# Performance work log

Hardware: AMD Instinct MI355X
Metric: run time of the kernel (lower is better)

## Reference

```python
import jax, jax.numpy as jnp
import numpy as np

N_FREQS = 10
EPS = 1e-5

def embed(p):
    # NeRF positional embedding: [p, sin(p*2^0), cos(p*2^0), ..., sin(p*2^9), cos(p*2^9)]
    freqs = 2.0 ** jnp.arange(N_FREQS, dtype=p.dtype)  # [10]
    ang = p[:, :, None] * freqs[None, None, :]          # [N,3,10]
    sc = jnp.stack([jnp.sin(ang), jnp.cos(ang)], axis=-1)  # [N,3,10,2]
    return jnp.concatenate([p, sc.reshape(p.shape[0], -1)], axis=-1)  # [N, 63]

def edge_conv(x, edge_index, w1, b1, w2, b2):
    src, dst = edge_index[0], edge_index[1]
    xi = x[dst]                                # target features [E, F]
    h = jnp.concatenate([xi, x[src] - xi], -1)  # [E, 2F]
    h = jax.nn.relu(h @ w1 + b1) @ w2 + b2      # [E, out]
    n = x.shape[0]
    s = jax.ops.segment_sum(h, dst, num_segments=n)
    cnt = jax.ops.segment_sum(jnp.ones((h.shape[0],), h.dtype), dst, num_segments=n)
    return s / jnp.clip(cnt, 1.0)[:, None]      # mean aggregation

def batch_norm(x, gamma, beta):
    mu = jnp.mean(x, axis=0)
    var = jnp.mean((x - mu) ** 2, axis=0)
    return (x - mu) * jax.lax.rsqrt(var + EPS) * gamma + beta

def distribute_features(features, face_indices, num_vertices):
    n, f = features.shape
    feat = features.reshape(n * 3, f // 3)
    idx = face_indices.reshape(-1)
    vsum = jax.ops.segment_sum(feat, idx, num_segments=num_vertices)
    cnt = jax.ops.segment_sum(jnp.ones((idx.shape[0],), feat.dtype), idx, num_segments=num_vertices)
    vmean = vsum / jnp.clip(cnt, 1.0)[:, None]
    return vmean[idx].reshape(n, f)

def _mlp_params(key, in_dim, out_dim):
    k1, k2, k3, k4 = jax.random.split(key, 4)
    h = 2 * out_dim
    return (jax.random.normal(k1, (2 * in_dim, h), jnp.float32) * (1.0 / np.sqrt(2 * in_dim)),
            jax.random.normal(k2, (h,), jnp.float32) * 0.01,
            jax.random.normal(k3, (h, out_dim), jnp.float32) * (1.0 / np.sqrt(h)),
            jax.random.normal(k4, (out_dim,), jnp.float32) * 0.01)

def setup_inputs() -> dict:
    key = jax.random.key(0)
    ks = jax.random.split(key, 10)
    N, E, V = 100000, 300000, 50000
    inp = {
        'x': jax.random.normal(ks[0], (N, 16), jnp.float32),
        'edge_index': jax.random.randint(ks[1], (2, E), 0, N, jnp.int32),
        'faces': jax.random.randint(ks[2], (N, 3), 0, V, jnp.int32),
        'num_vertices': V,
    }
    dims = [(196, 96), (96, 192), (192, 384), (384, 384), (384, 576)]
    for i, (di, do) in enumerate(dims, start=1):
        w1, b1, w2, b2 = _mlp_params(ks[2 + i], di, do)
        inp[f'gc{i}_w1'], inp[f'gc{i}_b1'], inp[f'gc{i}_w2'], inp[f'gc{i}_b2'] = w1, b1, w2, b2
    for i, d in enumerate([96, 192, 384, 384], start=1):
        inp[f'gamma{i}'] = jnp.ones((d,), jnp.float32)
        inp[f'beta{i}'] = jnp.zeros((d,), jnp.float32)
    return inp

def reference(x, edge_index, faces, num_vertices,
              gc1_w1, gc1_b1, gc1_w2, gc1_b2,
              gc2_w1, gc2_b1, gc2_w2, gc2_b2,
              gc3_w1, gc3_b1, gc3_w2, gc3_b2,
              gc4_w1, gc4_b1, gc4_w2, gc4_b2,
              gc5_w1, gc5_b1, gc5_w2, gc5_b2,
              gamma1, beta1, gamma2, beta2, gamma3, beta3, gamma4, beta4):
    h = jnp.concatenate([embed(x[:, :3]), embed(x[:, 3:6]), embed(x[:, 6:9]), x[:, 9:]], -1)  # [N,196]
    h = jax.nn.relu(batch_norm(edge_conv(h, edge_index, gc1_w1, gc1_b1, gc1_w2, gc1_b2), gamma1, beta1))
    h = distribute_features(h, faces, num_vertices)
    h = jax.nn.relu(batch_norm(edge_conv(h, edge_index, gc2_w1, gc2_b1, gc2_w2, gc2_b2), gamma2, beta2))
    h = distribute_features(h, faces, num_vertices)
    h = jax.nn.relu(batch_norm(edge_conv(h, edge_index, gc3_w1, gc3_b1, gc3_w2, gc3_b2), gamma3, beta3))
    h = distribute_features(h, faces, num_vertices)
    h = jax.nn.relu(batch_norm(edge_conv(h, edge_index, gc4_w1, gc4_b1, gc4_w2, gc4_b2), gamma4, beta4))
    h = distribute_features(h, faces, num_vertices)
    h = edge_conv(h, edge_index, gc5_w1, gc5_b1, gc5_w2, gc5_b2)
    h = distribute_features(h, faces, num_vertices)
    return h
```

## Files before the change

### kernel.cpp

```cpp
#include <hip/hip_runtime.h>
#include <hip/hip_bf16.h>
#include <stdint.h>


typedef __hip_bfloat16 bf16;
typedef __attribute__((ext_vector_type(8))) short bf16x8;
typedef __attribute__((ext_vector_type(4))) float f32x4;
#define CHUNK 384

static inline int cdiv(int a, int b) { return (a + b - 1) / b; }

__device__ __forceinline__ float bf2f(bf16 v) { return __bfloat162float(v); }
__device__ __forceinline__ bf16 f2bf(float v) { return __float2bfloat16(v); }
__device__ __forceinline__ unsigned short f2bs(float v) {
  bf16 h = __float2bfloat16(v);
  return *reinterpret_cast<unsigned short*>(&h);
}

__device__ __forceinline__ void gload16(const bf16* g, bf16* lds_base) {
  __builtin_amdgcn_global_load_lds((const __attribute__((address_space(1))) void*)g,
                                   (__attribute__((address_space(3))) void*)lds_base,
                                   16, 0, 0);
}

#define WAIT_VM0 asm volatile("s_waitcnt vmcnt(0)" ::: "memory")

__device__ __forceinline__ void swz_decode(int T, int nn, int& mb, int& nb) {
  int i = blockIdx.x;
  int q = T >> 3, r = T & 7;
  int xcd = i & 7, rank = i >> 3;
  int wg = (xcd < r ? xcd * (q + 1) : r * (q + 1) + (xcd - r) * q) + rank;
  nb = wg % nn;
  mb = wg / nn;
}

__global__ __launch_bounds__(256) void k_embed(const float* __restrict__ x,
                                               bf16* __restrict__ h, int N) {
  int idx = blockIdx.x * 256 + threadIdx.x;
  if (idx >= N * 224) return;
  int n = idx / 224;
  int c = idx - n * 224;
  float v = 0.f;
  if (c >= 196) {
    v = 0.f;
  } else if (c >= 189) {
    v = x[n * 16 + 9 + (c - 189)];
  } else {
    int g = c / 63;
    int cc = c - g * 63;
    const float* p = x + n * 16 + g * 3;
    if (cc < 3) {
      v = p[cc];
    } else {
      int t = cc - 3;
      int comp = t / 20;
      int rem = t - comp * 20;
      float ang = p[comp] * (float)(1 << (rem >> 1));
      v = (rem & 1) ? cosf(ang) : sinf(ang);
    }
  }
  h[idx] = f2bf(v);
}

__global__ __launch_bounds__(256) void k_count(const int* __restrict__ idxs,
                                               int* __restrict__ deg, int M) {
  int i = blockIdx.x * 256 + threadIdx.x;
  if (i < M) atomicAdd(&deg[idxs[i]], 1);
}

__global__ __launch_bounds__(256) void k_recip(const int* __restrict__ deg,
                                               float* __restrict__ r, int n) {
  int i = blockIdx.x * 256 + threadIdx.x;
  if (i < n) {
    int d = deg[i];
    r[i] = d > 0 ? 1.f / (float)d : 0.f;
  }
}

__global__ __launch_bounds__(1024) void k_scan(const int* __restrict__ deg,
                                               int* __restrict__ off,
                                               int* __restrict__ cursor, int n) {
  __shared__ int part[1024];
  int t = threadIdx.x;
  int per = (n + 1023) / 1024;
  int b = t * per;
  int e = b + per;
  if (b > n) b = n;
  if (e > n) e = n;
  int s = 0;
  for (int i = b; i < e; ++i) s += deg[i];
  part[t] = s;
  __syncthreads();
  if (t == 0) {
    int r = 0;
    for (int i = 0; i < 1024; ++i) {
      int x = part[i];
      part[i] = r;
      r += x;
    }
    off[n] = r;
  }
  __syncthreads();
  int r = part[t];
  for (int i = b; i < e; ++i) {
    off[i] = r;
    cursor[i] = r;
    r += deg[i];
  }
}

__global__ __launch_bounds__(256) void k_fill_edges(const int* __restrict__ ei, int E,
                                                    int* __restrict__ cursor,
                                                    int* __restrict__ esrc) {
  int e = blockIdx.x * 256 + threadIdx.x;
  if (e >= E) return;
  int dst = ei[E + e];
  int pos = atomicAdd(&cursor[dst], 1);
  esrc[pos] = ei[e];
}

__global__ __launch_bounds__(256) void k_fill_faces(const int* __restrict__ faces, int M,
                                                    int* __restrict__ cursor,
                                                    int* __restrict__ vidx) {
  int i = blockIdx.x * 256 + threadIdx.x;
  if (i >= M) return;
  int v = faces[i];
  int pos = atomicAdd(&cursor[v], 1);
  vidx[pos] = i;
}

__global__ __launch_bounds__(256) void k_prep_w1(const float* __restrict__ w1,
                                                 bf16* __restrict__ WdT,
                                                 bf16* __restrict__ WbT,
                                                 int F, int H, int F_pad, int H_pad) {
  int idx = blockIdx.x * 256 + threadIdx.x;
  if (idx >= H_pad * F_pad) return;
  int n = idx / F_pad;
  int k = idx - n * F_pad;
  float vd = 0.f, vb = 0.f;
  if (n < H && k < F) {
    float top = w1[(size_t)k * H + n];
    float bot = w1[(size_t)(F + k) * H + n];
    vd = top - bot;
    vb = bot;
  }
  WdT[idx] = f2bf(vd);
  WbT[idx] = f2bf(vb);
}

__global__ __launch_bounds__(256) void k_prep_w2(const float* __restrict__ w2,
                                                 bf16* __restrict__ W2T, int H, int O,
                                                 int O_pad) {
  int idx = blockIdx.x * 256 + threadIdx.x;
  if (idx >= O_pad * H) return;
  int n = idx / H;
  int k = idx - n * H;
  float v = (n < O) ? w2[(size_t)k * O + n] : 0.f;
  W2T[idx] = f2bf(v);
}

__global__ __launch_bounds__(256) void gemm1_mfma(
    const bf16* __restrict__ A, int lda,
    const bf16* __restrict__ WdT, const bf16* __restrict__ WbT,
    const float* __restrict__ b1, int c0,
    bf16* __restrict__ outC, bf16* __restrict__ outB,
    int N, int K_pad, int Hc, int nn) {
  __shared__ bf16 sA[2][128 * 32];
  __shared__ bf16 sBd[2][128 * 32];
  __shared__ bf16 sBb[2][128 * 32];
  int mb, nb;
  swz_decode(gridDim.x, nn, mb, nb);
  const int tid = threadIdx.x;
  const int lane = tid & 63, wv = tid >> 6;
  const int wm = wv & 1, wn = wv >> 1;
  const int lr = lane & 15, quad = lane >> 4;
  const int m_blk = mb * 128, n_blk = nb * 128;
  const int rs = lane >> 2;
  const int cg = (lane & 3) ^ ((lane >> 3) & 3);
  const int gsw = (quad ^ ((lr >> 1) & 3)) << 3;
  f32x4 accC[4][4], accB[4][4];
#pragma unroll
  for (int i = 0; i < 4; ++i)
#pragma unroll
    for (int j = 0; j < 4; ++j) {
      accC[i][j] = (f32x4){0.f, 0.f, 0.f, 0.f};
      accB[i][j] = (f32x4){0.f, 0.f, 0.f, 0.f};
    }

  auto stage = [&](int kt, int buf) {
    const int k0 = (kt << 5) + cg * 8;
#pragma unroll
    for (int i = 0; i < 2; ++i) {
      const int rb = wv * 32 + i * 16;
      const int ro = rb + rs;
      gload16(A + (size_t)(m_blk + ro) * lda + k0, &sA[buf][rb * 32]);
      gload16(WdT + (size_t)(n_blk + ro) * K_pad + k0, &sBd[buf][rb * 32]);
      gload16(WbT + (size_t)(n_blk + ro) * K_pad + k0, &sBb[buf][rb * 32]);
    }
  };
  auto compute = [&](int buf) {
    bf16x8 af[4];
#pragma unroll
    for (int im = 0; im < 4; ++im)
      af[im] = *(const bf16x8*)&sA[buf][(wm * 64 + im * 16 + lr) * 32 + gsw];
#pragma unroll
    for (int jn = 0; jn < 4; ++jn) {
      int go = (wn * 64 + jn * 16 + lr) * 32 + gsw;
      bf16x8 bd = *(const bf16x8*)&sBd[buf][go];
      bf16x8 bb = *(const bf16x8*)&sBb[buf][go];
#pragma unroll
      for (int im = 0; im < 4; ++im) {
        accC[im][jn] = __builtin_amdgcn_mfma_f32_16x16x32_bf16(af[im], bd, accC[im][jn], 0, 0, 0);
        accB[im][jn] = __builtin_amdgcn_mfma_f32_16x16x32_bf16(af[im], bb, accB[im][jn], 0, 0, 0);
      }
    }
  };

  const int kTiles = K_pad >> 5;
  stage(0, 0);
  WAIT_VM0;
  __builtin_amdgcn_s_barrier();
  int cur = 0;
  for (int kt = 0; kt < kTiles - 1; ++kt) {
    stage(kt + 1, cur ^ 1);
    compute(cur);
    WAIT_VM0;
    __builtin_amdgcn_s_barrier();
    cur ^= 1;
  }
  compute(cur);

#pragma unroll
  for (int jn = 0; jn < 4; ++jn) {
    int c = n_blk + wn * 64 + jn * 16 + lr;
    if (c >= Hc) continue;
    float bv = b1[c0 + c];
#pragma unroll
    for (int im = 0; im < 4; ++im) {
      int mb2 = m_blk + wm * 64 + im * 16 + quad * 4;
#pragma unroll
      for (int rg = 0; rg < 4; ++rg) {
        int r = mb2 + rg;
        if (r >= N) continue;
        size_t o = (size_t)r * Hc + c;
        outC[o] = f2bf(accC[im][jn][rg] + bv);
        outB[o] = f2bf(accB[im][jn][rg]);
      }
    }
  }
}

__global__ __launch_bounds__(256) void gemm2_mfma(
    const bf16* __restrict__ S, int ldS,
    const bf16* __restrict__ W2T, int ldw,
    const float* __restrict__ b2, const float* __restrict__ rdeg,
    float* __restrict__ Eo, float* __restrict__ stats, int do_stats,
    int N, int K, int O, int nn) {
  __shared__ bf16 sA[2][128 * 32];
  __shared__ bf16 sB[2][128 * 32];
  int mb, nb;
  swz_decode(gridDim.x, nn, mb, nb);
  const int tid = threadIdx.x;
  const int lane = tid & 63, wv = tid >> 6;
  const int wm = wv & 1, wn = wv >> 1;
  const int lr = lane & 15, quad = lane >> 4;
  const int m_blk = mb * 128, n_blk = nb * 128;
  const int rs = lane >> 2;
  const int cg = (lane & 3) ^ ((lane >> 3) & 3);
  const int gsw = (quad ^ ((lr >> 1) & 3)) << 3;
  f32x4 acc[4][4];
#pragma unroll
  for (int i = 0; i < 4; ++i)
#pragma unroll
    for (int j = 0; j < 4; ++j) acc[i][j] = (f32x4){0.f, 0.f, 0.f, 0.f};

  auto stage = [&](int kt, int buf) {
    const int k0 = (kt << 5) + cg * 8;
#pragma unroll
    for (int i = 0; i < 2; ++i) {
      const int rb = wv * 32 + i * 16;
      const int ro = rb + rs;
      gload16(S + (size_t)(m_blk + ro) * ldS + k0, &sA[buf][rb * 32]);
      gload16(W2T + (size_t)(n_blk + ro) * ldw + k0, &sB[buf][rb * 32]);
    }
  };
  auto compute = [&](int buf) {
    bf16x8 af[4];
#pragma unroll
    for (int im = 0; im < 4; ++im)
      af[im] = *(const bf16x8*)&sA[buf][(wm * 64 + im * 16 + lr) * 32 + gsw];
#pragma unroll
    for (int jn = 0; jn < 4; ++jn) {
      bf16x8 bb = *(const bf16x8*)&sB[buf][(wn * 64 + jn * 16 + lr) * 32 + gsw];
#pragma unroll
      for (int im = 0; im < 4; ++im)
        acc[im][jn] = __builtin_amdgcn_mfma_f32_16x16x32_bf16(af[im], bb, acc[im][jn], 0, 0, 0);
    }
  };

  const int kTiles = K >> 5;
  stage(0, 0);
  WAIT_VM0;
  __builtin_amdgcn_s_barrier();
  int cur = 0;
  for (int kt = 0; kt < kTiles - 1; ++kt) {
    stage(kt + 1, cur ^ 1);
    compute(cur);
    WAIT_VM0;
    __builtin_amdgcn_s_barrier();
    cur ^= 1;
  }
  compute(cur);

  float rdv[4][4];
#pragma unroll
  for (int im = 0; im < 4; ++im) {
    int mb2 = m_blk + wm * 64 + im * 16 + quad * 4;
#pragma unroll
    for (int rg = 0; rg < 4; ++rg) {
      int r = mb2 + rg;
      rdv[im][rg] = (r < N) ? rdeg[r] : 0.f;
    }
  }
#pragma unroll
  for (int jn = 0; jn < 4; ++jn) {
    int c = n_blk + wn * 64 + jn * 16 + lr;
    if (c >= O) continue;
    float b2v = b2[c];
    float ssum = 0.f, qsum = 0.f;
#pragma unroll
    for (int im = 0; im < 4; ++im) {
      int mb2 = m_blk + wm * 64 + im * 16 + quad * 4;
#pragma unroll
      for (int rg = 0; rg < 4; ++rg) {
        int r = mb2 + rg;
        if (r >= N) continue;
        float rd = rdv[im][rg];
        float v = acc[im][jn][rg] * rd;
        if (rd != 0.f) v += b2v;
        Eo[(size_t)r * O + c] = v;
        ssum += v;
        qsum += v * v;
      }
    }
    if (do_stats) {
      ssum += __shfl_xor(ssum, 16);
      ssum += __shfl_xor(ssum, 32);
      qsum += __shfl_xor(qsum, 16);
      qsum += __shfl_xor(qsum, 32);
      if (quad == 0) {
        unsafeAtomicAdd(&stats[c], ssum);
        unsafeAtomicAdd(&stats[O + c], qsum);
      }
    }
  }
}

__global__ __launch_bounds__(256) void k_edge_gather(
    const int* __restrict__ eoff, const int* __restrict__ esrc,
    const bf16* __restrict__ C, const bf16* __restrict__ B,
    bf16* __restrict__ S, int ldS, int c0, int N, int Hc) {
  int gw = (blockIdx.x * 256 + threadIdx.x) >> 6;
  int lane = threadIdx.x & 63;
  if (gw >= N) return;
  int beg = eoff[gw], end = eoff[gw + 1];
  const int nw = Hc >> 1;
  int j2w[3];
  float cc0[3], cc1[3], a0[3], a1[3];
  const uint32_t* Crow = reinterpret_cast<const uint32_t*>(C + (size_t)gw * Hc);
#pragma unroll
  for (int w = 0; w < 3; ++w) {
    j2w[w] = lane + w * 64;
    a0[w] = a1[w] = 0.f;
    cc0[w] = cc1[w] = 0.f;
    if (j2w[w] < nw) {
      uint32_t uc = Crow[j2w[w]];
      cc0[w] = __uint_as_float(uc << 16);
      cc1[w] = __uint_as_float(uc & 0xffff0000u);
    }
  }
  int e = beg;
  while (e < end) {
    int m = end - e;
    int take = (m < 3) ? m : 3;
    const uint32_t* R0 = reinterpret_cast<const uint32_t*>(B + (size_t)esrc[e] * Hc);
    const uint32_t* R1 =
        (take > 1) ? reinterpret_cast<const uint32_t*>(B + (size_t)esrc[e + 1] * Hc) : R0;
    const uint32_t* R2 =
        (take > 2) ? reinterpret_cast<const uint32_t*>(B + (size_t)esrc[e + 2] * Hc) : R0;
    uint32_t rA[3] = {0u, 0u, 0u}, rB_[3] = {0u, 0u, 0u}, rC_[3] = {0u, 0u, 0u};
#pragma unroll
    for (int w = 0; w < 3; ++w)
      if (j2w[w] < nw) rA[w] = R0[j2w[w]];
    if (take > 1) {
#pragma unroll
      for (int w = 0; w < 3; ++w)
        if (j2w[w] < nw) rB_[w] = R1[j2w[w]];
    }
    if (take > 2) {
#pragma unroll
      for (int w = 0; w < 3; ++w)
        if (j2w[w] < nw) rC_[w] = R2[j2w[w]];
    }
#pragma unroll
    for (int w = 0; w < 3; ++w) {
      a0[w] += fmaxf(cc0[w] + __uint_as_float(rA[w] << 16), 0.f);
      a1[w] += fmaxf(cc1[w] + __uint_as_float(rA[w] & 0xffff0000u), 0.f);
    }
    if (take > 1) {
#pragma unroll
      for (int w = 0; w < 3; ++w) {
        a0[w] += fmaxf(cc0[w] + __uint_as_float(rB_[w] << 16), 0.f);
        a1[w] += fmaxf(cc1[w] + __uint_as_float(rB_[w] & 0xffff0000u), 0.f);
      }
    }
    if (take > 2) {
#pragma unroll
      for (int w = 0; w < 3; ++w) {
        a0[w] += fmaxf(cc0[w] + __uint_as_float(rC_[w] << 16), 0.f);
        a1[w] += fmaxf(cc1[w] + __uint_as_float(rC_[w] & 0xffff0000u), 0.f);
      }
    }
    e += take;
  }
  uint32_t* Srow = reinterpret_cast<uint32_t*>(S + (size_t)gw * ldS + c0);
#pragma unroll
  for (int w = 0; w < 3; ++w)
    if (j2w[w] < nw)
      Srow[j2w[w]] = ((uint32_t)f2bs(a1[w]) << 16) | (uint32_t)f2bs(a0[w]);
}

__global__ __launch_bounds__(256) void k_bn_finalize(const float* __restrict__ stats,
                                                     const float* __restrict__ gamma,
                                                     const float* __restrict__ beta,
                                                     float* __restrict__ scale,
                                                     float* __restrict__ shift, int N, int O) {
  int c = blockIdx.x * 256 + threadIdx.x;
  if (c >= O) return;
  float mu = stats[c] / (float)N;
  float var = stats[O + c] / (float)N - mu * mu;
  float sc = gamma[c] * rsqrtf(var + 1e-5f);
  scale[c] = sc;
  shift[c] = beta[c] - mu * sc;
}

__global__ __launch_bounds__(256) void k_vgather(
    const int* __restrict__ voff, const int* __restrict__ vidx,
    const float* __restrict__ Ef, const float* __restrict__ scale,
    const float* __restrict__ shift, int use_bn,
    float* __restrict__ Vf, int V, int O, int O3) {
  int idx = blockIdx.x * 256 + threadIdx.x;
  if (idx >= V * O3) return;
  int v = idx / O3;
  int c = idx - v * O3;
  int beg = voff[v], end = voff[v + 1];
  float acc = 0.f;
  for (int e = beg; e < end; ++e) {
    int i = vidx[e];
    int n = i / 3;
    int g = i - n * 3;
    int col = g * O3 + c;
    float x = Ef[(size_t)n * O + col];
    if (use_bn) x = fmaxf(fmaf(x, scale[col], shift[col]), 0.f);
    acc += x;
  }
  Vf[idx] = acc;
}

__global__ __launch_bounds__(256) void k_gather_bf16(const float* __restrict__ Vf,
                                                     const int* __restrict__ faces,
                                                     const float* __restrict__ rv,
                                                     bf16* __restrict__ out,
                                                     int N, int O, int O3) {
  int idx = blockIdx.x * 256 + threadIdx.x;
  if (idx >= N * O) return;
  int n = idx / O;
  int c = idx - n * O;
  int g = c / O3;
  int vert = faces[n * 3 + g];
  out[idx] = f2bf(Vf[(size_t)vert * O3 + (c - g * O3)] * rv[vert]);
}

__global__ __launch_bounds__(256) void k_gather_f32(const float* __restrict__ Vf,
                                                    const int* __restrict__ faces,
                                                    const float* __restrict__ rv,
                                                    float* __restrict__ out,
                                                    int N, int O, int O3) {
  int idx = blockIdx.x * 256 + threadIdx.x;
  if (idx >= N * O) return;
  int n = idx / O;
  int c = idx - n * O;
  int g = c / O3;
  int vert = faces[n * 3 + g];
  out[idx] = Vf[(size_t)vert * O3 + (c - g * O3)] * rv[vert];
}

extern "C" void kernel_launch(void* const* d_in, const int* in_sizes, int n_in,
                              void* d_out, int out_size, void* d_ws, size_t ws_size,
                              hipStream_t stream) {
  (void)n_in; (void)out_size; (void)ws_size;
  const float* x = (const float*)d_in[0];
  const int* ei = (const int*)d_in[1];
  const int* faces = (const int*)d_in[2];
  const int N = in_sizes[0] / 16;
  const int E = in_sizes[1] / 2;
  const int V = 50000;
  const int N_pad = cdiv(N, 128) * 128;

  char* p = (char*)d_ws;
  auto carve = [&](size_t bytes) -> char* {
    char* r = p;
    p += (bytes + 255) & ~(size_t)255;
    return r;
  };
  bf16* buf_h = (bf16*)carve((size_t)N_pad * 384 * sizeof(bf16));
  float* buf_e = (float*)carve((size_t)N * 384 * sizeof(float));
  bf16* buf_C = (bf16*)carve((size_t)N * CHUNK * sizeof(bf16));
  bf16* buf_B = (bf16*)carve((size_t)N * CHUNK * sizeof(bf16));
  bf16* buf_S = (bf16*)carve((size_t)N_pad * 1152 * sizeof(bf16));
  float* buf_V = (float*)carve((size_t)V * 192 * sizeof(float));
  bf16* buf_WdT = (bf16*)carve((size_t)1050000 * sizeof(bf16));
  bf16* buf_WbT = (bf16*)carve((size_t)1050000 * sizeof(bf16));
  bf16* buf_W2T = (bf16*)carve((size_t)1500000 * sizeof(bf16));
  int* ideg = (int*)carve((size_t)N * 4);
  int* ivdeg = (int*)carve((size_t)V * 4);
  float* rdegN = (float*)carve((size_t)N * 4);
  float* rdegV = (float*)carve((size_t)V * 4);
  float* stats = (float*)carve(2 * 576 * 4);
  float* scale = (float*)carve(576 * 4);
  float* shift = (float*)carve(576 * 4);
  int* e_off = (int*)carve((size_t)(N + 1) * 4);
  int* e_cur = (int*)carve((size_t)N * 4);
  int* e_src = (int*)carve((size_t)E * 4);
  int* v_off = (int*)carve((size_t)(V + 1) * 4);
  int* v_cur = (int*)carve((size_t)V * 4);
  int* v_idx = (int*)carve((size_t)3 * N * 4);

  hipMemsetAsync(ideg, 0, (size_t)N * 4, stream);
  hipMemsetAsync(ivdeg, 0, (size_t)V * 4, stream);
  k_count<<<cdiv(E, 256), 256, 0, stream>>>(ei + E, ideg, E);
  k_count<<<cdiv(3 * N, 256), 256, 0, stream>>>(faces, ivdeg, 3 * N);
  k_recip<<<cdiv(N, 256), 256, 0, stream>>>(ideg, rdegN, N);
  k_recip<<<cdiv(V, 256), 256, 0, stream>>>(ivdeg, rdegV, V);

  k_scan<<<1, 1024, 0, stream>>>(ideg, e_off, e_cur, N);
  k_scan<<<1, 1024, 0, stream>>>(ivdeg, v_off, v_cur, V);
  k_fill_edges<<<cdiv(E, 256), 256, 0, stream>>>(ei, E, e_cur, e_src);
  k_fill_faces<<<cdiv(3 * N, 256), 256, 0, stream>>>(faces, 3 * N, v_cur, v_idx);

  k_embed<<<cdiv(N * 224, 256), 256, 0, stream>>>(x, buf_h, N);

  const int LF[5] = {196, 96, 192, 384, 384};
  const int LH[5] = {192, 384, 768, 768, 1152};
  const int LO[5] = {96, 192, 384, 384, 576};

  size_t off1 = 0, off2 = 0;
  const int nm = cdiv(N, 128);

  for (int l = 0; l < 5; ++l) {
    const int F = LF[l], H = LH[l], O = LO[l], O3 = O / 3;
    const int F_pad = ((F + 31) / 32) * 32;
    int Hc_last = H % CHUNK;
    if (Hc_last == 0) Hc_last = CHUNK;
    const int H_pad = H - Hc_last + cdiv(Hc_last, 128) * 128;
    const int O_pad = cdiv(O, 128) * 128;
    const float* w1 = (const float*)d_in[4 + l * 4];
    const float* b1 = (const float*)d_in[5 + l * 4];
    const float* w2 = (const float*)d_in[6 + l * 4];
    const float* b2 = (const float*)d_in[7 + l * 4];
    float* Ebuf = (l == 4) ? (float*)d_out : buf_e;
    bf16* WdT = buf_WdT + off1;
    bf16* WbT = buf_WbT + off1;
    bf16* W2T = buf_W2T + off2;
    off1 += (size_t)H_pad * F_pad;
    off2 += (size_t)O_pad * H;

    k_prep_w1<<<cdiv(H_pad * F_pad, 256), 256, 0, stream>>>(w1, WdT, WbT, F, H, F_pad, H_pad);
    k_prep_w2<<<cdiv(O_pad * H, 256), 256, 0, stream>>>(w2, W2T, H, O, O_pad);

    for (int c0 = 0; c0 < H; c0 += CHUNK) {
      int Hc = (H - c0 < CHUNK) ? (H - c0) : CHUNK;
      int nn1 = cdiv(Hc, 128);
      gemm1_mfma<<<nm * nn1, 256, 0, stream>>>(buf_h, F_pad,
                                               WdT + (size_t)c0 * F_pad, WbT + (size_t)c0 * F_pad,
                                               b1, c0, buf_C, buf_B, N, F_pad, Hc, nn1);
      k_edge_gather<<<cdiv(N * 64, 256), 256, 0, stream>>>(e_off, e_src, buf_C, buf_B,
                                                           buf_S, H, c0, N, Hc);
    }

    if (l < 4) hipMemsetAsync(stats, 0, (size_t)2 * O * 4, stream);
    int nn2 = cdiv(O, 128);
    gemm2_mfma<<<nm * nn2, 256, 0, stream>>>(buf_S, H, W2T, H, b2, rdegN, Ebuf,
                                             stats, (l < 4) ? 1 : 0, N, H, O, nn2);

    if (l < 4)
      k_bn_finalize<<<cdiv(O, 256), 256, 0, stream>>>(
          stats, (const float*)d_in[24 + l * 2], (const float*)d_in[25 + l * 2],
          scale, shift, N, O);

    k_vgather<<<cdiv(V * O3, 256), 256, 0, stream>>>(v_off, v_idx, Ebuf, scale, shift,
                                                     (l < 4) ? 1 : 0, buf_V, V, O, O3);
    if (l < 4)
      k_gather_bf16<<<cdiv(N * O, 256), 256, 0, stream>>>(buf_V, faces, rdegV, buf_h, N, O, O3);
    else
      k_gather_f32<<<cdiv(N * O, 256), 256, 0, stream>>>(buf_V, faces, rdegV, (float*)d_out, N, O, O3);
  }
}
```

Measured before the change: 4.282 ms.

## Triple-buffer gemm2 K-loop and store intermediate edge outputs in bf16

The second GEMM's K loop moves from double-buffered to triple-buffered LDS staging, using partial vmcnt waits so that two tiles of loads stay in flight during compute. For layers 1-4, the GEMM2 output (pre-batchnorm) is now written as bf16 instead of fp32, which halves the write and the later vertex-gather read traffic. The vertex gather is split into a bf16 variant with BN+ReLU and an fp32 variant for the final layer. The trade-offs are extra LDS use, which may lower occupancy, an added barrier per K step, and bf16 rounding of intermediate activations. BN statistics are still accumulated from the fp32 values.

```diff
diff --git a/kernel.cpp b/kernel.cpp
--- a/kernel.cpp
+++ b/kernel.cpp
@@ -23,7 +23,7 @@
                                    16, 0, 0);
 }
 
-#define WAIT_VM0 asm volatile("s_waitcnt vmcnt(0)" ::: "memory")
+#define WAIT_VM(N) asm volatile("s_waitcnt vmcnt(" #N ")" ::: "memory")
 
 __device__ __forceinline__ void swz_decode(int T, int nn, int& mb, int& nb) {
   int i = blockIdx.x;
@@ -218,13 +218,13 @@
 
   const int kTiles = K_pad >> 5;
   stage(0, 0);
-  WAIT_VM0;
+  WAIT_VM(0);
   __builtin_amdgcn_s_barrier();
   int cur = 0;
   for (int kt = 0; kt < kTiles - 1; ++kt) {
     stage(kt + 1, cur ^ 1);
     compute(cur);
-    WAIT_VM0;
+    WAIT_VM(0);
     __builtin_amdgcn_s_barrier();
     cur ^= 1;
   }
@@ -254,10 +254,11 @@
     const bf16* __restrict__ S, int ldS,
     const bf16* __restrict__ W2T, int ldw,
     const float* __restrict__ b2, const float* __restrict__ rdeg,
-    float* __restrict__ Eo, float* __restrict__ stats, int do_stats,
+    float* __restrict__ Eo32, bf16* __restrict__ Eo16, int out_bf16,
+    float* __restrict__ stats, int do_stats,
     int N, int K, int O, int nn) {
-  __shared__ bf16 sA[2][128 * 32];
-  __shared__ bf16 sB[2][128 * 32];
+  __shared__ bf16 sA[3][128 * 32];
+  __shared__ bf16 sB[3][128 * 32];
   int mb, nb;
   swz_decode(gridDim.x, nn, mb, nb);
   const int tid = threadIdx.x;
@@ -300,17 +301,21 @@
 
   const int kTiles = K >> 5;
   stage(0, 0);
-  WAIT_VM0;
-  __builtin_amdgcn_s_barrier();
-  int cur = 0;
-  for (int kt = 0; kt < kTiles - 1; ++kt) {
-    stage(kt + 1, cur ^ 1);
-    compute(cur);
-    WAIT_VM0;
+  stage(1, 1);
+  for (int kt = 0; kt < kTiles; ++kt) {
+    if (kt + 2 < kTiles) {
+      int t2 = kt + 2;
+      stage(t2, t2 - (t2 / 3) * 3);
+      WAIT_VM(8);
+    } else if (kt + 1 < kTiles) {
+      WAIT_VM(4);
+    } else {
+      WAIT_VM(0);
+    }
     __builtin_amdgcn_s_barrier();
-    cur ^= 1;
-  }
-  compute(cur);
+    compute(kt - (kt / 3) * 3);
+    __builtin_amdgcn_s_barrier();
+  }
 
   float rdv[4][4];
 #pragma unroll
@@ -338,7 +343,9 @@
         float rd = rdv[im][rg];
         float v = acc[im][jn][rg] * rd;
         if (rd != 0.f) v += b2v;
-        Eo[(size_t)r * O + c] = v;
+        size_t o = (size_t)r * O + c;
+        if (out_bf16) Eo16[o] = f2bf(v);
+        else Eo32[o] = v;
         ssum += v;
         qsum += v * v;
       }
@@ -444,10 +451,10 @@
   shift[c] = beta[c] - mu * sc;
 }
 
-__global__ __launch_bounds__(256) void k_vgather(
+__global__ __launch_bounds__(256) void k_vgather_bf16(
     const int* __restrict__ voff, const int* __restrict__ vidx,
-    const float* __restrict__ Ef, const float* __restrict__ scale,
-    const float* __restrict__ shift, int use_bn,
+    const bf16* __restrict__ Ef, const float* __restrict__ scale,
+    const float* __restrict__ shift,
     float* __restrict__ Vf, int V, int O, int O3) {
   int idx = blockIdx.x * 256 + threadIdx.x;
   if (idx >= V * O3) return;
@@ -460,9 +467,27 @@
     int n = i / 3;
     int g = i - n * 3;
     int col = g * O3 + c;
-    float x = Ef[(size_t)n * O + col];
-    if (use_bn) x = fmaxf(fmaf(x, scale[col], shift[col]), 0.f);
-    acc += x;
+    float x = bf2f(Ef[(size_t)n * O + col]);
+    acc += fmaxf(fmaf(x, scale[col], shift[col]), 0.f);
+  }
+  Vf[idx] = acc;
+}
+
+__global__ __launch_bounds__(256) void k_vgather_f32(
+    const int* __restrict__ voff, const int* __restrict__ vidx,
+    const float* __restrict__ Ef,
+    float* __restrict__ Vf, int V, int O, int O3) {
+  int idx = blockIdx.x * 256 + threadIdx.x;
+  if (idx >= V * O3) return;
+  int v = idx / O3;
+  int c = idx - v * O3;
+  int beg = voff[v], end = voff[v + 1];
+  float acc = 0.f;
+  for (int e = beg; e < end; ++e) {
+    int i = vidx[e];
+    int n = i / 3;
+    int g = i - n * 3;
+    acc += Ef[(size_t)n * O + g * O3 + c];
   }
   Vf[idx] = acc;
 }
@@ -514,7 +539,7 @@
     return r;
   };
   bf16* buf_h = (bf16*)carve((size_t)N_pad * 384 * sizeof(bf16));
-  float* buf_e = (float*)carve((size_t)N * 384 * sizeof(float));
+  bf16* buf_eo = (bf16*)carve((size_t)N * 384 * sizeof(bf16));
   bf16* buf_C = (bf16*)carve((size_t)N * CHUNK * sizeof(bf16));
   bf16* buf_B = (bf16*)carve((size_t)N * CHUNK * sizeof(bf16));
   bf16* buf_S = (bf16*)carve((size_t)N_pad * 1152 * sizeof(bf16));
@@ -568,7 +593,6 @@
     const float* b1 = (const float*)d_in[5 + l * 4];
     const float* w2 = (const float*)d_in[6 + l * 4];
     const float* b2 = (const float*)d_in[7 + l * 4];
-    float* Ebuf = (l == 4) ? (float*)d_out : buf_e;
     bf16* WdT = buf_WdT + off1;
     bf16* WbT = buf_WbT + off1;
     bf16* W2T = buf_W2T + off2;
@@ -590,19 +614,23 @@
 
     if (l < 4) hipMemsetAsync(stats, 0, (size_t)2 * O * 4, stream);
     int nn2 = cdiv(O, 128);
-    gemm2_mfma<<<nm * nn2, 256, 0, stream>>>(buf_S, H, W2T, H, b2, rdegN, Ebuf,
+    gemm2_mfma<<<nm * nn2, 256, 0, stream>>>(buf_S, H, W2T, H, b2, rdegN,
+                                             (l == 4) ? (float*)d_out : nullptr,
+                                             (l < 4) ? buf_eo : nullptr,
+                                             (l < 4) ? 1 : 0,
                                              stats, (l < 4) ? 1 : 0, N, H, O, nn2);
 
-    if (l < 4)
+    if (l < 4) {
       k_bn_finalize<<<cdiv(O, 256), 256, 0, stream>>>(
           stats, (const float*)d_in[24 + l * 2], (const float*)d_in[25 + l * 2],
           scale, shift, N, O);
-
-    k_vgather<<<cdiv(V * O3, 256), 256, 0, stream>>>(v_off, v_idx, Ebuf, scale, shift,
-                                                     (l < 4) ? 1 : 0, buf_V, V, O, O3);
-    if (l < 4)
+      k_vgather_bf16<<<cdiv(V * O3, 256), 256, 0, stream>>>(v_off, v_idx, buf_eo, scale,
+                                                            shift, buf_V, V, O, O3);
       k_gather_bf16<<<cdiv(N * O, 256), 256, 0, stream>>>(buf_V, faces, rdegV, buf_h, N, O, O3);
-    else
+    } else {
+      k_vgather_f32<<<cdiv(V * O3, 256), 256, 0, stream>>>(v_off, v_idx, (const float*)d_out,
+                                                           buf_V, V, O, O3);
       k_gather_f32<<<cdiv(N * O, 256), 256, 0, stream>>>(buf_V, faces, rdegV, (float*)d_out, N, O, O3);
-  }
-}
+    }
+  }
+}
```

New measurement: 4.312 ms. Within noise of the previous version (+0.7%).
